# Kernel optimization log

Measured on AMD Instinct MI355X. Metric: run time of the kernel, lower is better.

Reference implementation:

```python
import jax, jax.numpy as jnp
import numpy as np

# Dimensions
B, T, IN = 8, 64, 6       # batch, timesteps, strain components
G = 256                   # grain_num
H = 32                    # hidden_dim (units)
W = 128                   # quadratic block width
OUT = 3                   # output_dim
DEPTH = 4                 # quadratic block depth
SD = H + IN               # start_dim = units + in_channels = 38
EPS = 1e-15


def setup_inputs() -> dict:
    key = jax.random.key(0)
    ks = jax.random.split(key, 24)
    s = 0.08  # xavier-ish scale for width-128 linears
    d = {
        "x": jax.random.normal(ks[0], (B, T, IN), dtype=jnp.float32),
        "init_ori": jax.random.normal(ks[1], (B, G, 3), dtype=jnp.float32),
        # Quadratic block branch A (modlist1): first layer SD->W, then (DEPTH-1) W->W
        "qbA_W0": jax.random.normal(ks[2], (SD, W)) * s,
        "qbA_b0": jnp.zeros((W,), jnp.float32),
        "qbA_Ws": jax.random.normal(ks[3], (DEPTH - 1, W, W)) * s,
        "qbA_bs": jnp.zeros((DEPTH - 1, W), jnp.float32),
        # Quadratic block branch B (modlist2)
        "qbB_W0": jax.random.normal(ks[4], (SD, W)) * s,
        "qbB_b0": jnp.zeros((W,), jnp.float32),
        "qbB_Ws": jax.random.normal(ks[5], (DEPTH - 1, W, W)) * s,
        "qbB_bs": jnp.zeros((DEPTH - 1, W), jnp.float32),
        # fc_alpha: W -> H ; fc_beta (1-layer DNN): W -> H
        "alpha_W": jax.random.normal(ks[6], (W, H)) * s,
        "alpha_b": jnp.zeros((H,), jnp.float32),
        "beta_W": jax.random.normal(ks[7], (W, H)) * s,
        "beta_b": jnp.zeros((H,), jnp.float32),
        # nn_out DNN: layers = [H, 128, 128, OUT], tanh between hidden layers
        "out_W0": jax.random.normal(ks[8], (H, 128)) * s,
        "out_b0": jnp.zeros((128,), jnp.float32),
        "out_W1": jax.random.normal(ks[9], (128, 128)) * s,
        "out_b1": jnp.zeros((128,), jnp.float32),
        "out_W2": jax.random.normal(ks[10], (128, OUT)) * s,
        "out_b2": jnp.zeros((OUT,), jnp.float32),
    }
    return d


def reference(x, init_ori, qbA_W0, qbA_b0, qbA_Ws, qbA_bs,
              qbB_W0, qbB_b0, qbB_Ws, qbB_bs,
              alpha_W, alpha_b, beta_W, beta_b,
              out_W0, out_b0, out_W1, out_b1, out_W2, out_b2):
    b = x.shape[0]
    # h0 = zeros with first 3 hidden channels set to initial orientations
    h0 = jnp.zeros((b, G, H), x.dtype).at[:, :, :3].set(init_ori)

    def step(h, x_t):  # h: [B,G,H], x_t: [B,IN]
        sn = jnp.linalg.norm(x_t, axis=-1, keepdims=True)          # [B,1]
        xn = x_t / (sn + EPS)                                      # normalized strain direction
        z = jnp.concatenate(
            [jnp.broadcast_to(xn[:, None, :], (b, G, IN)), h], axis=-1)  # [B,G,SD]
        # quadratic block: elementwise product of two linear branches
        a = jnp.tanh(z @ qbA_W0 + qbA_b0)
        c = jnp.tanh(z @ qbB_W0 + qbB_b0)
        z = a * c
        for j in range(DEPTH - 1):
            a = z @ qbA_Ws[j] + qbA_bs[j]
            c = z @ qbB_Ws[j] + qbB_bs[j]
            if j < DEPTH - 2:  # tanh on all but the last quadratic layer
                a = jnp.tanh(a)
                c = jnp.tanh(c)
            z = a * c
        q = jnp.tanh(z)                                            # [B,G,W]
        alpha = jnp.exp(q @ alpha_W + alpha_b)                     # [B,G,H]
        beta = jnp.tanh(q @ beta_W + beta_b)                       # [B,G,H]
        decay = jnp.exp(-alpha * sn[:, :, None])                   # exp(-alpha*||strain||)
        h_new = decay * (h - beta) + beta                          # gated state update
        # nn_out DNN [H,128,128,OUT] with tanh hidden activations
        o = jnp.tanh(h_new @ out_W0 + out_b0)
        o = jnp.tanh(o @ out_W1 + out_b1)
        o = o @ out_W2 + out_b2                                    # [B,G,OUT]
        return h_new, o

    _, outs = jax.lax.scan(step, h0, jnp.swapaxes(x, 0, 1))        # outs: [T,B,G,OUT]
    return jnp.transpose(outs, (1, 2, 0, 3))                       # [B,G,T,OUT]
```

## Files before the change

### kernel.cpp

```cpp
#include <hip/hip_runtime.h>

typedef _Float16 f16;
typedef _Float16 f16x4 __attribute__((ext_vector_type(4)));
typedef _Float16 f16x8 __attribute__((ext_vector_type(8)));
typedef float f32x4 __attribute__((ext_vector_type(4)));
typedef unsigned int u32;

#define MFMA16(a,b,c) __builtin_amdgcn_mfma_f32_16x16x32_f16(a,b,c,0,0,0)

#define BAR() asm volatile("s_waitcnt lgkmcnt(0)\n\ts_barrier" ::: "memory")

#define OFF_A0 0
#define OFF_B0 8192
#define OFF_AW 16384
#define OFF_BW 65536
#define OFF_AL 114688
#define OFF_BE 118784
#define OFF_O0 122880
#define OFF_O1 126976
#define OFF_O2 143360
#define PACK_TOTAL 145408
#define OFF_HH 262144

struct PackSrcs { const float* p[9]; };

__global__ __launch_bounds__(256) void pack_all(PackSrcs ps, f16* __restrict__ dst){
  int idx = blockIdx.x*256 + threadIdx.x;
  if (idx >= PACK_TOTAL) return;
  const float* src; int base, Kreal, Nreal, KT;
  if (idx < 16384){
    if (idx < 8192){ src=ps.p[0]; base=0; } else { src=ps.p[1]; base=8192; }
    Kreal=38; Nreal=128; KT=2;
  } else if (idx < 65536){
    int s=(idx-16384)>>14; src=ps.p[2]+s*16384; base=16384+s*16384; Kreal=128; Nreal=128; KT=4;
  } else if (idx < 114688){
    int s=(idx-65536)>>14; src=ps.p[3]+s*16384; base=65536+s*16384; Kreal=128; Nreal=128; KT=4;
  } else if (idx < 122880){
    if (idx<118784){ src=ps.p[4]; base=114688; } else { src=ps.p[5]; base=118784; }
    Kreal=128; Nreal=32; KT=4;
  } else if (idx < 126976){
    src=ps.p[6]; base=122880; Kreal=32; Nreal=128; KT=1;
  } else if (idx < 143360){
    src=ps.p[7]; base=126976; Kreal=128; Nreal=128; KT=4;
  } else {
    src=ps.p[8]; base=143360; Kreal=128; Nreal=3; KT=4;
  }
  int local = idx - base;
  int j = local & 7, lane = (local>>3)&63, rem = local>>9;
  int kt = rem % KT, nt = rem / KT;
  int k = kt*32 + ((lane>>4)<<3) + j;
  int n = nt*16 + (lane&15);
  dst[idx] = (f16)((k<Kreal && n<Nreal) ? src[k*Nreal+n] : 0.f);
}

__device__ __forceinline__ float tanhfast(float x){
  float e = __builtin_amdgcn_exp2f(x * 2.885390082f);
  return 1.f - 2.f*__builtin_amdgcn_rcpf(e + 1.f);
}
__device__ __forceinline__ float expfast(float x){
  return __builtin_amdgcn_exp2f(x * 1.44269504f);
}

__device__ __forceinline__ f16x8 ldW(const f16* wp, int off, int KT, int nt, int kt, int l){
  return *(const f16x8*)(wp + off + (((nt*KT + kt)*64 + l)<<3));
}

template<int LAST>
__device__ __forceinline__ void qphase(const f16* __restrict__ Zi, f16* __restrict__ Zo,
                                       const f16x8 (&WA)[4], const f16x8 (&WB)[4],
                                       const float* __restrict__ bA,
                                       const float* __restrict__ bB,
                                       int l, int d0, int n16){
  f16x8 Bq[4];
#pragma unroll
  for (int kt=0; kt<4; ++kt) Bq[kt] = *(const f16x8*)(Zi + ((kt*64 + l)<<3));
  f32x4 a = *(const f32x4*)(bA + d0);
  f32x4 c = *(const f32x4*)(bB + d0);
#pragma unroll
  for (int kt=0; kt<4; ++kt){
    a = MFMA16(WA[kt], Bq[kt], a);
    c = MFMA16(WB[kt], Bq[kt], c);
  }
  f16x4 z4;
#pragma unroll
  for (int i=0;i<4;++i){
    float z = LAST ? tanhfast(a[i]*c[i]) : tanhfast(a[i])*tanhfast(c[i]);
    z4[i] = (f16)z;
  }
  int kt_o = d0>>5, lane_o = (((d0&31)>>3)<<4) | n16, j0 = d0&7;
  *(f16x4*)(Zo + ((kt_o*64 + lane_o)<<3) + j0) = z4;
}

__global__ __launch_bounds__(512,2)
void lmsc_rec(const float* __restrict__ x, const float* __restrict__ init_ori,
              const f16* __restrict__ wp,
              const float* __restrict__ ba0, const float* __restrict__ bas,
              const float* __restrict__ bb0, const float* __restrict__ bbs,
              const float* __restrict__ b_al, const float* __restrict__ b_be,
              f16* __restrict__ hG)
{
  __shared__ __align__(16) f16 S[2][1024];
  __shared__ __align__(16) f16 Z[2][2048];
  __shared__ float biasA[4][128], biasB[4][128], biasAB[64];
  __shared__ float hbuf[512];
  __shared__ float xnL[64][8];

  const int tid = (int)threadIdx.x;
  const int l = tid & 63, wid = tid >> 6;
  const int n16 = l & 15, rhi = l >> 4;
  const int d0 = (wid<<4) + (rhi<<2);
  const int tile = (int)blockIdx.x, b = tile >> 4, Rbase = tile << 4;

  f16x8 w0A[2], w0B[2];
#pragma unroll
  for (int kt=0;kt<2;++kt){
    w0A[kt] = ldW(wp, OFF_A0, 2, wid, kt, l);
    w0B[kt] = ldW(wp, OFF_B0, 2, wid, kt, l);
  }
  f16x8 wqA[3][4], wqB[3][4];
#pragma unroll
  for (int ly=0;ly<3;++ly)
#pragma unroll
    for (int kt=0;kt<4;++kt){
      wqA[ly][kt] = ldW(wp, OFF_AW + ly*16384, 4, wid, kt, l);
      wqB[ly][kt] = ldW(wp, OFF_BW + ly*16384, 4, wid, kt, l);
    }
  f16x8 wal[4], wbe[4];
  if (wid < 2){
#pragma unroll
    for (int kt=0;kt<4;++kt){
      wal[kt] = ldW(wp, OFF_AL, 4, wid, kt, l);
      wbe[kt] = ldW(wp, OFF_BE, 4, wid, kt, l);
    }
  }

  ((u32*)S)[tid] = 0u; ((u32*)S)[tid+512] = 0u;
  if (tid < 128){
    biasA[0][tid] = ba0[tid]; biasB[0][tid] = bb0[tid];
#pragma unroll
    for (int j=0;j<3;++j){ biasA[1+j][tid] = bas[j*128+tid]; biasB[1+j][tid] = bbs[j*128+tid]; }
  }
  if (tid < 32){ biasAB[tid] = b_al[tid]; biasAB[32+tid] = b_be[tid]; }
  if (tid < 64){
    const float* xp = x + (b*64 + tid)*6;
    float s2 = 0.f;
#pragma unroll
    for (int i=0;i<6;++i) s2 += xp[i]*xp[i];
    float sn = sqrtf(s2);
    float inv = 1.f/(sn + 1e-15f);
#pragma unroll
    for (int i=0;i<6;++i) xnL[tid][i] = xp[i]*inv;
    xnL[tid][6] = sn;
  }
  __syncthreads();
  if (tid < 256){
    int r = tid & 15, cc = tid >> 4;
#pragma unroll
    for (int e=0;e<2;++e){
      int c = cc + e*16;
      float h0 = (c < 3) ? init_ori[(Rbase + r)*3 + c] : 0.f;
      hbuf[c*16 + r] = h0;
      f16 hh = (f16)h0, hl = (f16)(h0 - (float)hh);
      int k = 6 + c;
      int idx = (((k>>5)*64 + (((k&31)>>3)<<4) + r)<<3) + (k&7);
      S[0][idx] = hh; S[1][idx] = hl;
    }
  }
  if (tid < 96){
    int r2 = tid/6, c2 = tid - r2*6;
    float xv = xnL[0][c2];
    f16 xh = (f16)xv, xl = (f16)(xv - (float)xh);
    S[0][(r2<<3)+c2] = xh; S[1][(r2<<3)+c2] = xl;
  }
  __syncthreads();

  for (int t=0; t<64; ++t){
    {
      f16x8 Bh[2], Bl[2];
#pragma unroll
      for (int kt=0;kt<2;++kt){
        Bh[kt] = *(const f16x8*)(&S[0][(kt*64+l)<<3]);
        Bl[kt] = *(const f16x8*)(&S[1][(kt*64+l)<<3]);
      }
      f32x4 aH = *(const f32x4*)(&biasA[0][d0]);
      f32x4 cH = *(const f32x4*)(&biasB[0][d0]);
      f32x4 aL = {0,0,0,0}, cL = {0,0,0,0};
#pragma unroll
      for (int kt=0;kt<2;++kt){
        aH = MFMA16(w0A[kt], Bh[kt], aH); aL = MFMA16(w0A[kt], Bl[kt], aL);
        cH = MFMA16(w0B[kt], Bh[kt], cH); cL = MFMA16(w0B[kt], Bl[kt], cL);
      }
      f16x4 z4;
#pragma unroll
      for (int i=0;i<4;++i)
        z4[i] = (f16)(tanhfast(aH[i]+aL[i]) * tanhfast(cH[i]+cL[i]));
      int kt_o = d0>>5, lane_o = (((d0&31)>>3)<<4) | n16, j0 = d0&7;
      *(f16x4*)(&Z[0][((kt_o*64 + lane_o)<<3) + j0]) = z4;
    }
    BAR();
    qphase<0>(Z[0], Z[1], wqA[0], wqB[0], biasA[1], biasB[1], l, d0, n16);
    BAR();
    qphase<0>(Z[1], Z[0], wqA[1], wqB[1], biasA[2], biasB[2], l, d0, n16);
    BAR();
    qphase<1>(Z[0], Z[1], wqA[2], wqB[2], biasA[3], biasB[3], l, d0, n16);
    BAR();
    if (wid < 2){
      f16x8 q[4];
#pragma unroll
      for (int kt=0;kt<4;++kt) q[kt] = *(const f16x8*)(&Z[1][(kt*64+l)<<3]);
      f32x4 ua = *(const f32x4*)(&biasAB[d0]);
      f32x4 ub = *(const f32x4*)(&biasAB[32+d0]);
#pragma unroll
      for (int kt=0;kt<4;++kt){
        ua = MFMA16(wal[kt], q[kt], ua);
        ub = MFMA16(wbe[kt], q[kt], ub);
      }
      float sn = xnL[t][6];
      int mt = tile*64 + t;
      f16x4 hh4;
#pragma unroll
      for (int i=0;i<4;++i){
        float alv = expfast(fminf(ua[i], 80.f));
        float bev = tanhfast(ub[i]);
        int c = d0 + i;
        float hold = hbuf[c*16 + n16];
        float hn = __builtin_amdgcn_exp2f(-1.44269504f*alv*sn)*(hold - bev) + bev;
        hbuf[c*16 + n16] = hn;
        f16 hh = (f16)hn; hh4[i] = hh;
        if (t < 63){
          f16 hl = (f16)(hn - (float)hh);
          int k = 6 + c;
          int idx = (((k>>5)*64 + (((k&31)>>3)<<4) + n16)<<3) + (k&7);
          S[0][idx] = hh; S[1][idx] = hl;
        }
      }
      int lane_o = ((d0>>3)<<4) | n16;
      *(f16x4*)(hG + mt*512 + lane_o*8 + (d0&7)) = hh4;
    }
    if (t < 63 && tid >= 384 && tid < 480){
      int i2 = tid - 384;
      int r2 = i2/6, c2 = i2 - r2*6;
      float xv = xnL[t+1][c2];
      f16 xh = (f16)xv, xl = (f16)(xv - (float)xh);
      S[0][(r2<<3)+c2] = xh; S[1][(r2<<3)+c2] = xl;
    }
    BAR();
  }
}

__global__ __launch_bounds__(512,4)
void lmsc_out(const f16* __restrict__ wp, const f16* __restrict__ hG,
              const float* __restrict__ bo0, const float* __restrict__ bo1,
              const float* __restrict__ bo2, float* __restrict__ out)
{
  __shared__ __align__(16) f16 o1b[16384];
  __shared__ __align__(16) f16 o2b[16384];
  const int tid=(int)threadIdx.x, l=tid&63, wid=tid>>6;
  const int n16=l&15, rhi=l>>4;
  const int mtb = (int)blockIdx.x * 8;
  f16x8 W0a = ldW(wp, OFF_O0, 1, wid, 0, l);
  f16x8 W1a[4], W2a[4];
#pragma unroll
  for (int kt=0;kt<4;++kt){ W1a[kt]=ldW(wp,OFF_O1,4,wid,kt,l); W2a[kt]=ldW(wp,OFF_O2,4,0,kt,l); }
  const int d0 = wid*16 + rhi*4;
  const f32x4 b0v = *(const f32x4*)(bo0 + d0);
  const f32x4 b1v = *(const f32x4*)(bo1 + d0);
  const int kt_o = d0>>5, lane_o = (((d0&31)>>3)<<4) + n16, j0 = d0&7;
#pragma unroll
  for (int s=0;s<8;++s){
    int mt = mtb + s;
    f16x8 Bh = *(const f16x8*)(hG + ((mt*64+l)<<3));
    f32x4 acc = b0v;
    acc = MFMA16(W0a, Bh, acc);
    f16x4 z4;
#pragma unroll
    for (int i=0;i<4;++i) z4[i] = (f16)tanhfast(acc[i]);
    *(f16x4*)(&o1b[(((s*4+kt_o)*64 + lane_o)<<3) + j0]) = z4;
  }
  __syncthreads();
#pragma unroll
  for (int s=0;s<8;++s){
    f32x4 acc = b1v;
#pragma unroll
    for (int kt=0;kt<4;++kt){
      f16x8 B = *(const f16x8*)(&o1b[((s*4+kt)*64 + l)<<3]);
      acc = MFMA16(W1a[kt], B, acc);
    }
    f16x4 z4;
#pragma unroll
    for (int i=0;i<4;++i) z4[i] = (f16)tanhfast(acc[i]);
    *(f16x4*)(&o2b[(((s*4+kt_o)*64 + lane_o)<<3) + j0]) = z4;
  }
  __syncthreads();
  {
    f32x4 acc = {0,0,0,0};
#pragma unroll
    for (int kt=0;kt<4;++kt){
      f16x8 B = *(const f16x8*)(&o2b[((wid*4+kt)*64 + l)<<3]);
      acc = MFMA16(W2a[kt], B, acc);
    }
    if (l < 16){
      int mt = mtb + wid, grow = (mt>>6)*16 + n16, tt = mt & 63;
#pragma unroll
      for (int i=0;i<3;++i)
        out[(grow*64 + tt)*3 + i] = acc[i] + bo2[i];
    }
  }
}

extern "C" void kernel_launch(void* const* d_in, const int* in_sizes, int n_in,
                              void* d_out, int out_size, void* d_ws, size_t ws_size,
                              hipStream_t stream){
  const float* x        = (const float*)d_in[0];
  const float* init_ori = (const float*)d_in[1];
  f16* wp = (f16*)d_ws;

  PackSrcs ps;
  ps.p[0] = (const float*)d_in[2];
  ps.p[1] = (const float*)d_in[6];
  ps.p[2] = (const float*)d_in[4];
  ps.p[3] = (const float*)d_in[8];
  ps.p[4] = (const float*)d_in[10];
  ps.p[5] = (const float*)d_in[12];
  ps.p[6] = (const float*)d_in[14];
  ps.p[7] = (const float*)d_in[16];
  ps.p[8] = (const float*)d_in[18];
  pack_all<<<(PACK_TOTAL+255)/256, 256, 0, stream>>>(ps, wp);

  lmsc_rec<<<128,512,0,stream>>>(x, init_ori, wp,
      (const float*)d_in[3],  (const float*)d_in[5],
      (const float*)d_in[7],  (const float*)d_in[9],
      (const float*)d_in[11], (const float*)d_in[13],
      wp + OFF_HH);
  lmsc_out<<<1024,512,0,stream>>>(wp, wp + OFF_HH,
      (const float*)d_in[15], (const float*)d_in[17], (const float*)d_in[19],
      (float*)d_out);
}
```

Baseline: 139.7 us.

## Split MFMA accumulation chains, fuse tanh products, keep hidden state in registers

The 4-deep dependent MFMA chains in the quadratic layers and the alpha/beta projection are split into two independent accumulator chains that are summed at the end, which shortens the dependency latency on the serial recurrence path. The product of two tanh values is computed from two exp2 calls and a single reciprocal instead of two reciprocals. The recurrent hidden state moves from an LDS buffer into per-thread registers, removing an LDS read and write each step. Risks include extra VGPR pressure under the 512x2 launch bounds and a slight change in rounding from the exp clamping and the reordered summation.

New measurement: 151.9 us. 8.8% more time.

```diff
diff --git a/kernel.cpp b/kernel.cpp
--- a/kernel.cpp
+++ b/kernel.cpp
@@ -60,6 +60,13 @@
 __device__ __forceinline__ float expfast(float x){
   return __builtin_amdgcn_exp2f(x * 1.44269504f);
 }
+__device__ __forceinline__ float tanh2prod(float a, float c){
+  float pa = __builtin_amdgcn_exp2f(fminf(a*2.885390082f, 60.f));
+  float pc = __builtin_amdgcn_exp2f(fminf(c*2.885390082f, 60.f));
+  float num = (pa-1.f)*(pc-1.f);
+  float den = (pa+1.f)*(pc+1.f);
+  return num * __builtin_amdgcn_rcpf(den);
+}
 
 __device__ __forceinline__ f16x8 ldW(const f16* wp, int off, int KT, int nt, int kt, int l){
   return *(const f16x8*)(wp + off + (((nt*KT + kt)*64 + l)<<3));
@@ -74,17 +81,18 @@
   f16x8 Bq[4];
 #pragma unroll
   for (int kt=0; kt<4; ++kt) Bq[kt] = *(const f16x8*)(Zi + ((kt*64 + l)<<3));
-  f32x4 a = *(const f32x4*)(bA + d0);
-  f32x4 c = *(const f32x4*)(bB + d0);
-#pragma unroll
-  for (int kt=0; kt<4; ++kt){
-    a = MFMA16(WA[kt], Bq[kt], a);
-    c = MFMA16(WB[kt], Bq[kt], c);
-  }
+  f32x4 a0 = *(const f32x4*)(bA + d0);
+  f32x4 c0 = *(const f32x4*)(bB + d0);
+  f32x4 a1 = {0,0,0,0}, c1 = {0,0,0,0};
+  a0 = MFMA16(WA[0], Bq[0], a0); c0 = MFMA16(WB[0], Bq[0], c0);
+  a1 = MFMA16(WA[2], Bq[2], a1); c1 = MFMA16(WB[2], Bq[2], c1);
+  a0 = MFMA16(WA[1], Bq[1], a0); c0 = MFMA16(WB[1], Bq[1], c0);
+  a1 = MFMA16(WA[3], Bq[3], a1); c1 = MFMA16(WB[3], Bq[3], c1);
+  f32x4 a = a0 + a1, c = c0 + c1;
   f16x4 z4;
 #pragma unroll
   for (int i=0;i<4;++i){
-    float z = LAST ? tanhfast(a[i]*c[i]) : tanhfast(a[i])*tanhfast(c[i]);
+    float z = LAST ? tanhfast(a[i]*c[i]) : tanh2prod(a[i], c[i]);
     z4[i] = (f16)z;
   }
   int kt_o = d0>>5, lane_o = (((d0&31)>>3)<<4) | n16, j0 = d0&7;
@@ -102,7 +110,6 @@
   __shared__ __align__(16) f16 S[2][1024];
   __shared__ __align__(16) f16 Z[2][2048];
   __shared__ float biasA[4][128], biasB[4][128], biasAB[64];
-  __shared__ float hbuf[512];
   __shared__ float xnL[64][8];
 
   const int tid = (int)threadIdx.x;
@@ -152,6 +159,14 @@
     for (int i=0;i<6;++i) xnL[tid][i] = xp[i]*inv;
     xnL[tid][6] = sn;
   }
+  float hreg[4] = {0.f,0.f,0.f,0.f};
+  if (wid < 2){
+#pragma unroll
+    for (int i=0;i<4;++i){
+      int c = d0 + i;
+      hreg[i] = (c < 3) ? init_ori[(Rbase + n16)*3 + c] : 0.f;
+    }
+  }
   __syncthreads();
   if (tid < 256){
     int r = tid & 15, cc = tid >> 4;
@@ -159,7 +174,6 @@
     for (int e=0;e<2;++e){
       int c = cc + e*16;
       float h0 = (c < 3) ? init_ori[(Rbase + r)*3 + c] : 0.f;
-      hbuf[c*16 + r] = h0;
       f16 hh = (f16)h0, hl = (f16)(h0 - (float)hh);
       int k = 6 + c;
       int idx = (((k>>5)*64 + (((k&31)>>3)<<4) + r)<<3) + (k&7);
@@ -193,7 +207,7 @@
       f16x4 z4;
 #pragma unroll
       for (int i=0;i<4;++i)
-        z4[i] = (f16)(tanhfast(aH[i]+aL[i]) * tanhfast(cH[i]+cL[i]));
+        z4[i] = (f16)tanh2prod(aH[i]+aL[i], cH[i]+cL[i]);
       int kt_o = d0>>5, lane_o = (((d0&31)>>3)<<4) | n16, j0 = d0&7;
       *(f16x4*)(&Z[0][((kt_o*64 + lane_o)<<3) + j0]) = z4;
     }
@@ -208,13 +222,14 @@
       f16x8 q[4];
 #pragma unroll
       for (int kt=0;kt<4;++kt) q[kt] = *(const f16x8*)(&Z[1][(kt*64+l)<<3]);
-      f32x4 ua = *(const f32x4*)(&biasAB[d0]);
-      f32x4 ub = *(const f32x4*)(&biasAB[32+d0]);
-#pragma unroll
-      for (int kt=0;kt<4;++kt){
-        ua = MFMA16(wal[kt], q[kt], ua);
-        ub = MFMA16(wbe[kt], q[kt], ub);
-      }
+      f32x4 ua0 = *(const f32x4*)(&biasAB[d0]);
+      f32x4 ub0 = *(const f32x4*)(&biasAB[32+d0]);
+      f32x4 ua1 = {0,0,0,0}, ub1 = {0,0,0,0};
+      ua0 = MFMA16(wal[0], q[0], ua0); ub0 = MFMA16(wbe[0], q[0], ub0);
+      ua1 = MFMA16(wal[2], q[2], ua1); ub1 = MFMA16(wbe[2], q[2], ub1);
+      ua0 = MFMA16(wal[1], q[1], ua0); ub0 = MFMA16(wbe[1], q[1], ub0);
+      ua1 = MFMA16(wal[3], q[3], ua1); ub1 = MFMA16(wbe[3], q[3], ub1);
+      f32x4 ua = ua0 + ua1, ub = ub0 + ub1;
       float sn = xnL[t][6];
       int mt = tile*64 + t;
       f16x4 hh4;
@@ -223,9 +238,8 @@
         float alv = expfast(fminf(ua[i], 80.f));
         float bev = tanhfast(ub[i]);
         int c = d0 + i;
-        float hold = hbuf[c*16 + n16];
-        float hn = __builtin_amdgcn_exp2f(-1.44269504f*alv*sn)*(hold - bev) + bev;
-        hbuf[c*16 + n16] = hn;
+        float hn = __builtin_amdgcn_exp2f(-1.44269504f*alv*sn)*(hreg[i] - bev) + bev;
+        hreg[i] = hn;
         f16 hh = (f16)hn; hh4[i] = hh;
         if (t < 63){
           f16 hl = (f16)(hn - (float)hh);
```

## Fuse recurrence and output MLP into one kernel with flag-based producer-consumer overlap

Applied to the files above, without the earlier changes.

Merges the recurrent kernel and the output MLP kernel into one launch of 256 blocks. The first 128 blocks run the recurrence and release a global atomic flag after every 8 timesteps. The other 128 blocks spin on those flags and run the output MLP on each finished chunk while the recurrence continues. This hides the output-MLP work and one launch behind the serial recurrence, but it relies on all 256 blocks being resident at once and adds larger shared memory per block plus the cost of spin-waiting.

After: 171.0 us. 22.5% more time.

```diff
diff --git a/kernel.cpp b/kernel.cpp
--- a/kernel.cpp
+++ b/kernel.cpp
@@ -20,13 +20,15 @@
 #define OFF_O1 126976
 #define OFF_O2 143360
 #define PACK_TOTAL 145408
+#define FLAG_ELEM 153600
 #define OFF_HH 262144
 
 struct PackSrcs { const float* p[9]; };
 
 __global__ __launch_bounds__(256) void pack_all(PackSrcs ps, f16* __restrict__ dst){
   int idx = blockIdx.x*256 + threadIdx.x;
-  if (idx >= PACK_TOTAL) return;
+  if (idx >= PACK_TOTAL + 1024) return;
+  if (idx >= PACK_TOTAL){ ((u32*)(dst + FLAG_ELEM))[idx - PACK_TOTAL] = 0u; return; }
   const float* src; int base, Kreal, Nreal, KT;
   if (idx < 16384){
     if (idx < 8192){ src=ps.p[0]; base=0; } else { src=ps.p[1]; base=8192; }
@@ -92,218 +94,229 @@
 }
 
 __global__ __launch_bounds__(512,2)
-void lmsc_rec(const float* __restrict__ x, const float* __restrict__ init_ori,
-              const f16* __restrict__ wp,
-              const float* __restrict__ ba0, const float* __restrict__ bas,
-              const float* __restrict__ bb0, const float* __restrict__ bbs,
-              const float* __restrict__ b_al, const float* __restrict__ b_be,
-              f16* __restrict__ hG)
+void lmsc_fused(const float* __restrict__ x, const float* __restrict__ init_ori,
+                const f16* __restrict__ wp,
+                const float* __restrict__ ba0, const float* __restrict__ bas,
+                const float* __restrict__ bb0, const float* __restrict__ bbs,
+                const float* __restrict__ b_al, const float* __restrict__ b_be,
+                const float* __restrict__ bo0, const float* __restrict__ bo1,
+                const float* __restrict__ bo2,
+                f16* __restrict__ hG, u32* __restrict__ flags,
+                float* __restrict__ out)
 {
   __shared__ __align__(16) f16 S[2][1024];
   __shared__ __align__(16) f16 Z[2][2048];
   __shared__ float biasA[4][128], biasB[4][128], biasAB[64];
   __shared__ float hbuf[512];
   __shared__ float xnL[64][8];
+  __shared__ __align__(16) f16 o1b[16384];
+  __shared__ __align__(16) f16 o2b[16384];
 
   const int tid = (int)threadIdx.x;
   const int l = tid & 63, wid = tid >> 6;
   const int n16 = l & 15, rhi = l >> 4;
-  const int d0 = (wid<<4) + (rhi<<2);
-  const int tile = (int)blockIdx.x, b = tile >> 4, Rbase = tile << 4;
-
-  f16x8 w0A[2], w0B[2];
-#pragma unroll
-  for (int kt=0;kt<2;++kt){
-    w0A[kt] = ldW(wp, OFF_A0, 2, wid, kt, l);
-    w0B[kt] = ldW(wp, OFF_B0, 2, wid, kt, l);
-  }
-  f16x8 wqA[3][4], wqB[3][4];
-#pragma unroll
-  for (int ly=0;ly<3;++ly)
-#pragma unroll
-    for (int kt=0;kt<4;++kt){
-      wqA[ly][kt] = ldW(wp, OFF_AW + ly*16384, 4, wid, kt, l);
-      wqB[ly][kt] = ldW(wp, OFF_BW + ly*16384, 4, wid, kt, l);
-    }
-  f16x8 wal[4], wbe[4];
-  if (wid < 2){
-#pragma unroll
-    for (int kt=0;kt<4;++kt){
-      wal[kt] = ldW(wp, OFF_AL, 4, wid, kt, l);
-      wbe[kt] = ldW(wp, OFF_BE, 4, wid, kt, l);
-    }
-  }
-
-  ((u32*)S)[tid] = 0u; ((u32*)S)[tid+512] = 0u;
-  if (tid < 128){
-    biasA[0][tid] = ba0[tid]; biasB[0][tid] = bb0[tid];
-#pragma unroll
-    for (int j=0;j<3;++j){ biasA[1+j][tid] = bas[j*128+tid]; biasB[1+j][tid] = bbs[j*128+tid]; }
-  }
-  if (tid < 32){ biasAB[tid] = b_al[tid]; biasAB[32+tid] = b_be[tid]; }
-  if (tid < 64){
-    const float* xp = x + (b*64 + tid)*6;
-    float s2 = 0.f;
-#pragma unroll
-    for (int i=0;i<6;++i) s2 += xp[i]*xp[i];
-    float sn = sqrtf(s2);
-    float inv = 1.f/(sn + 1e-15f);
-#pragma unroll
-    for (int i=0;i<6;++i) xnL[tid][i] = xp[i]*inv;
-    xnL[tid][6] = sn;
-  }
-  __syncthreads();
-  if (tid < 256){
-    int r = tid & 15, cc = tid >> 4;
-#pragma unroll
-    for (int e=0;e<2;++e){
-      int c = cc + e*16;
-      float h0 = (c < 3) ? init_ori[(Rbase + r)*3 + c] : 0.f;
-      hbuf[c*16 + r] = h0;
-      f16 hh = (f16)h0, hl = (f16)(h0 - (float)hh);
-      int k = 6 + c;
-      int idx = (((k>>5)*64 + (((k&31)>>3)<<4) + r)<<3) + (k&7);
-      S[0][idx] = hh; S[1][idx] = hl;
-    }
-  }
-  if (tid < 96){
-    int r2 = tid/6, c2 = tid - r2*6;
-    float xv = xnL[0][c2];
-    f16 xh = (f16)xv, xl = (f16)(xv - (float)xh);
-    S[0][(r2<<3)+c2] = xh; S[1][(r2<<3)+c2] = xl;
-  }
-  __syncthreads();
-
-  for (int t=0; t<64; ++t){
-    {
-      f16x8 Bh[2], Bl[2];
-#pragma unroll
-      for (int kt=0;kt<2;++kt){
-        Bh[kt] = *(const f16x8*)(&S[0][(kt*64+l)<<3]);
-        Bl[kt] = *(const f16x8*)(&S[1][(kt*64+l)<<3]);
-      }
-      f32x4 aH = *(const f32x4*)(&biasA[0][d0]);
-      f32x4 cH = *(const f32x4*)(&biasB[0][d0]);
-      f32x4 aL = {0,0,0,0}, cL = {0,0,0,0};
-#pragma unroll
-      for (int kt=0;kt<2;++kt){
-        aH = MFMA16(w0A[kt], Bh[kt], aH); aL = MFMA16(w0A[kt], Bl[kt], aL);
-        cH = MFMA16(w0B[kt], Bh[kt], cH); cL = MFMA16(w0B[kt], Bl[kt], cL);
-      }
-      f16x4 z4;
-#pragma unroll
-      for (int i=0;i<4;++i)
-        z4[i] = (f16)(tanhfast(aH[i]+aL[i]) * tanhfast(cH[i]+cL[i]));
-      int kt_o = d0>>5, lane_o = (((d0&31)>>3)<<4) | n16, j0 = d0&7;
-      *(f16x4*)(&Z[0][((kt_o*64 + lane_o)<<3) + j0]) = z4;
-    }
-    BAR();
-    qphase<0>(Z[0], Z[1], wqA[0], wqB[0], biasA[1], biasB[1], l, d0, n16);
-    BAR();
-    qphase<0>(Z[1], Z[0], wqA[1], wqB[1], biasA[2], biasB[2], l, d0, n16);
-    BAR();
-    qphase<1>(Z[0], Z[1], wqA[2], wqB[2], biasA[3], biasB[3], l, d0, n16);
-    BAR();
+
+  if (blockIdx.x < 128){
+    const int d0 = (wid<<4) + (rhi<<2);
+    const int tile = (int)blockIdx.x, b = tile >> 4, Rbase = tile << 4;
+
+    f16x8 w0A[2], w0B[2];
+#pragma unroll
+    for (int kt=0;kt<2;++kt){
+      w0A[kt] = ldW(wp, OFF_A0, 2, wid, kt, l);
+      w0B[kt] = ldW(wp, OFF_B0, 2, wid, kt, l);
+    }
+    f16x8 wqA[3][4], wqB[3][4];
+#pragma unroll
+    for (int ly=0;ly<3;++ly)
+#pragma unroll
+      for (int kt=0;kt<4;++kt){
+        wqA[ly][kt] = ldW(wp, OFF_AW + ly*16384, 4, wid, kt, l);
+        wqB[ly][kt] = ldW(wp, OFF_BW + ly*16384, 4, wid, kt, l);
+      }
+    f16x8 wal[4], wbe[4];
     if (wid < 2){
-      f16x8 q[4];
-#pragma unroll
-      for (int kt=0;kt<4;++kt) q[kt] = *(const f16x8*)(&Z[1][(kt*64+l)<<3]);
-      f32x4 ua = *(const f32x4*)(&biasAB[d0]);
-      f32x4 ub = *(const f32x4*)(&biasAB[32+d0]);
 #pragma unroll
       for (int kt=0;kt<4;++kt){
-        ua = MFMA16(wal[kt], q[kt], ua);
-        ub = MFMA16(wbe[kt], q[kt], ub);
-      }
-      float sn = xnL[t][6];
-      int mt = tile*64 + t;
-      f16x4 hh4;
-#pragma unroll
-      for (int i=0;i<4;++i){
-        float alv = expfast(fminf(ua[i], 80.f));
-        float bev = tanhfast(ub[i]);
-        int c = d0 + i;
-        float hold = hbuf[c*16 + n16];
-        float hn = __builtin_amdgcn_exp2f(-1.44269504f*alv*sn)*(hold - bev) + bev;
-        hbuf[c*16 + n16] = hn;
-        f16 hh = (f16)hn; hh4[i] = hh;
-        if (t < 63){
-          f16 hl = (f16)(hn - (float)hh);
-          int k = 6 + c;
-          int idx = (((k>>5)*64 + (((k&31)>>3)<<4) + n16)<<3) + (k&7);
-          S[0][idx] = hh; S[1][idx] = hl;
-        }
-      }
-      int lane_o = ((d0>>3)<<4) | n16;
-      *(f16x4*)(hG + mt*512 + lane_o*8 + (d0&7)) = hh4;
-    }
-    if (t < 63 && tid >= 384 && tid < 480){
-      int i2 = tid - 384;
-      int r2 = i2/6, c2 = i2 - r2*6;
-      float xv = xnL[t+1][c2];
+        wal[kt] = ldW(wp, OFF_AL, 4, wid, kt, l);
+        wbe[kt] = ldW(wp, OFF_BE, 4, wid, kt, l);
+      }
+    }
+
+    ((u32*)S)[tid] = 0u; ((u32*)S)[tid+512] = 0u;
+    if (tid < 128){
+      biasA[0][tid] = ba0[tid]; biasB[0][tid] = bb0[tid];
+#pragma unroll
+      for (int j=0;j<3;++j){ biasA[1+j][tid] = bas[j*128+tid]; biasB[1+j][tid] = bbs[j*128+tid]; }
+    }
+    if (tid < 32){ biasAB[tid] = b_al[tid]; biasAB[32+tid] = b_be[tid]; }
+    if (tid < 64){
+      const float* xp = x + (b*64 + tid)*6;
+      float s2 = 0.f;
+#pragma unroll
+      for (int i=0;i<6;++i) s2 += xp[i]*xp[i];
+      float sn = sqrtf(s2);
+      float inv = 1.f/(sn + 1e-15f);
+#pragma unroll
+      for (int i=0;i<6;++i) xnL[tid][i] = xp[i]*inv;
+      xnL[tid][6] = sn;
+    }
+    __syncthreads();
+    if (tid < 256){
+      int r = tid & 15, cc = tid >> 4;
+#pragma unroll
+      for (int e=0;e<2;++e){
+        int c = cc + e*16;
+        float h0 = (c < 3) ? init_ori[(Rbase + r)*3 + c] : 0.f;
+        hbuf[c*16 + r] = h0;
+        f16 hh = (f16)h0, hl = (f16)(h0 - (float)hh);
+        int k = 6 + c;
+        int idx = (((k>>5)*64 + (((k&31)>>3)<<4) + r)<<3) + (k&7);
+        S[0][idx] = hh; S[1][idx] = hl;
+      }
+    }
+    if (tid < 96){
+      int r2 = tid/6, c2 = tid - r2*6;
+      float xv = xnL[0][c2];
       f16 xh = (f16)xv, xl = (f16)(xv - (float)xh);
       S[0][(r2<<3)+c2] = xh; S[1][(r2<<3)+c2] = xl;
     }
-    BAR();
-  }
-}
-
-__global__ __launch_bounds__(512,4)
-void lmsc_out(const f16* __restrict__ wp, const f16* __restrict__ hG,
-              const float* __restrict__ bo0, const float* __restrict__ bo1,
-              const float* __restrict__ bo2, float* __restrict__ out)
-{
-  __shared__ __align__(16) f16 o1b[16384];
-  __shared__ __align__(16) f16 o2b[16384];
-  const int tid=(int)threadIdx.x, l=tid&63, wid=tid>>6;
-  const int n16=l&15, rhi=l>>4;
-  const int mtb = (int)blockIdx.x * 8;
-  f16x8 W0a = ldW(wp, OFF_O0, 1, wid, 0, l);
-  f16x8 W1a[4], W2a[4];
-#pragma unroll
-  for (int kt=0;kt<4;++kt){ W1a[kt]=ldW(wp,OFF_O1,4,wid,kt,l); W2a[kt]=ldW(wp,OFF_O2,4,0,kt,l); }
-  const int d0 = wid*16 + rhi*4;
-  const f32x4 b0v = *(const f32x4*)(bo0 + d0);
-  const f32x4 b1v = *(const f32x4*)(bo1 + d0);
-  const int kt_o = d0>>5, lane_o = (((d0&31)>>3)<<4) + n16, j0 = d0&7;
-#pragma unroll
-  for (int s=0;s<8;++s){
-    int mt = mtb + s;
-    f16x8 Bh = *(const f16x8*)(hG + ((mt*64+l)<<3));
-    f32x4 acc = b0v;
-    acc = MFMA16(W0a, Bh, acc);
-    f16x4 z4;
-#pragma unroll
-    for (int i=0;i<4;++i) z4[i] = (f16)tanhfast(acc[i]);
-    *(f16x4*)(&o1b[(((s*4+kt_o)*64 + lane_o)<<3) + j0]) = z4;
-  }
-  __syncthreads();
-#pragma unroll
-  for (int s=0;s<8;++s){
-    f32x4 acc = b1v;
-#pragma unroll
-    for (int kt=0;kt<4;++kt){
-      f16x8 B = *(const f16x8*)(&o1b[((s*4+kt)*64 + l)<<3]);
-      acc = MFMA16(W1a[kt], B, acc);
-    }
-    f16x4 z4;
-#pragma unroll
-    for (int i=0;i<4;++i) z4[i] = (f16)tanhfast(acc[i]);
-    *(f16x4*)(&o2b[(((s*4+kt_o)*64 + lane_o)<<3) + j0]) = z4;
-  }
-  __syncthreads();
-  {
-    f32x4 acc = {0,0,0,0};
-#pragma unroll
-    for (int kt=0;kt<4;++kt){
-      f16x8 B = *(const f16x8*)(&o2b[((wid*4+kt)*64 + l)<<3]);
-      acc = MFMA16(W2a[kt], B, acc);
-    }
-    if (l < 16){
-      int mt = mtb + wid, grow = (mt>>6)*16 + n16, tt = mt & 63;
-#pragma unroll
-      for (int i=0;i<3;++i)
-        out[(grow*64 + tt)*3 + i] = acc[i] + bo2[i];
+    __syncthreads();
+
+    for (int t=0; t<64; ++t){
+      {
+        f16x8 Bh[2], Bl[2];
+#pragma unroll
+        for (int kt=0;kt<2;++kt){
+          Bh[kt] = *(const f16x8*)(&S[0][(kt*64+l)<<3]);
+          Bl[kt] = *(const f16x8*)(&S[1][(kt*64+l)<<3]);
+        }
+        f32x4 aH = *(const f32x4*)(&biasA[0][d0]);
+        f32x4 cH = *(const f32x4*)(&biasB[0][d0]);
+        f32x4 aL = {0,0,0,0}, cL = {0,0,0,0};
+#pragma unroll
+        for (int kt=0;kt<2;++kt){
+          aH = MFMA16(w0A[kt], Bh[kt], aH); aL = MFMA16(w0A[kt], Bl[kt], aL);
+          cH = MFMA16(w0B[kt], Bh[kt], cH); cL = MFMA16(w0B[kt], Bl[kt], cL);
+        }
+        f16x4 z4;
+#pragma unroll
+        for (int i=0;i<4;++i)
+          z4[i] = (f16)(tanhfast(aH[i]+aL[i]) * tanhfast(cH[i]+cL[i]));
+        int kt_o = d0>>5, lane_o = (((d0&31)>>3)<<4) | n16, j0 = d0&7;
+        *(f16x4*)(&Z[0][((kt_o*64 + lane_o)<<3) + j0]) = z4;
+      }
+      BAR();
+      qphase<0>(Z[0], Z[1], wqA[0], wqB[0], biasA[1], biasB[1], l, d0, n16);
+      BAR();
+      qphase<0>(Z[1], Z[0], wqA[1], wqB[1], biasA[2], biasB[2], l, d0, n16);
+      BAR();
+      qphase<1>(Z[0], Z[1], wqA[2], wqB[2], biasA[3], biasB[3], l, d0, n16);
+      BAR();
+      if (wid < 2){
+        f16x8 q[4];
+#pragma unroll
+        for (int kt=0;kt<4;++kt) q[kt] = *(const f16x8*)(&Z[1][(kt*64+l)<<3]);
+        f32x4 ua = *(const f32x4*)(&biasAB[d0]);
+        f32x4 ub = *(const f32x4*)(&biasAB[32+d0]);
+#pragma unroll
+        for (int kt=0;kt<4;++kt){
+          ua = MFMA16(wal[kt], q[kt], ua);
+          ub = MFMA16(wbe[kt], q[kt], ub);
+        }
+        float sn = xnL[t][6];
+        int mt = tile*64 + t;
+        f16x4 hh4;
+#pragma unroll
+        for (int i=0;i<4;++i){
+          float alv = expfast(fminf(ua[i], 80.f));
+          float bev = tanhfast(ub[i]);
+          int c = d0 + i;
+          float hold = hbuf[c*16 + n16];
+          float hn = __builtin_amdgcn_exp2f(-1.44269504f*alv*sn)*(hold - bev) + bev;
+          hbuf[c*16 + n16] = hn;
+          f16 hh = (f16)hn; hh4[i] = hh;
+          if (t < 63){
+            f16 hl = (f16)(hn - (float)hh);
+            int k = 6 + c;
+            int idx = (((k>>5)*64 + (((k&31)>>3)<<4) + n16)<<3) + (k&7);
+            S[0][idx] = hh; S[1][idx] = hl;
+          }
+        }
+        int lane_o = ((d0>>3)<<4) | n16;
+        *(f16x4*)(hG + mt*512 + lane_o*8 + (d0&7)) = hh4;
+        if ((t & 7) == 7 && l == 0)
+          __hip_atomic_fetch_add(&flags[(tile<<3) + (t>>3)], 1u,
+                                 __ATOMIC_RELEASE, __HIP_MEMORY_SCOPE_AGENT);
+      }
+      if (t < 63 && tid >= 384 && tid < 480){
+        int i2 = tid - 384;
+        int r2 = i2/6, c2 = i2 - r2*6;
+        float xv = xnL[t+1][c2];
+        f16 xh = (f16)xv, xl = (f16)(xv - (float)xh);
+        S[0][(r2<<3)+c2] = xh; S[1][(r2<<3)+c2] = xl;
+      }
+      BAR();
+    }
+  } else {
+    const int r = (int)blockIdx.x - 128;
+    f16x8 W0a = ldW(wp, OFF_O0, 1, wid, 0, l);
+    f16x8 W1a[4], W2a[4];
+#pragma unroll
+    for (int kt=0;kt<4;++kt){ W1a[kt]=ldW(wp,OFF_O1,4,wid,kt,l); W2a[kt]=ldW(wp,OFF_O2,4,0,kt,l); }
+    const int d0 = wid*16 + rhi*4;
+    const f32x4 b0v = *(const f32x4*)(bo0 + d0);
+    const f32x4 b1v = *(const f32x4*)(bo1 + d0);
+    const int kt_o = d0>>5, lane_o = (((d0&31)>>3)<<4) + n16, j0 = d0&7;
+    u32* fl = flags + (r<<3);
+
+    for (int oct=0; oct<8; ++oct){
+      if (tid == 0){
+        while (__hip_atomic_load(&fl[oct], __ATOMIC_ACQUIRE, __HIP_MEMORY_SCOPE_AGENT) < 2u)
+          __builtin_amdgcn_s_sleep(4);
+      }
+      __syncthreads();
+      const int mtb = (r<<6) + (oct<<3);
+#pragma unroll
+      for (int s=0;s<8;++s){
+        int mt = mtb + s;
+        f16x8 Bh = *(const f16x8*)(hG + ((mt*64+l)<<3));
+        f32x4 acc = b0v;
+        acc = MFMA16(W0a, Bh, acc);
+        f16x4 z4;
+#pragma unroll
+        for (int i=0;i<4;++i) z4[i] = (f16)tanhfast(acc[i]);
+        *(f16x4*)(&o1b[(((s*4+kt_o)*64 + lane_o)<<3) + j0]) = z4;
+      }
+      __syncthreads();
+#pragma unroll
+      for (int s=0;s<8;++s){
+        f32x4 acc = b1v;
+#pragma unroll
+        for (int kt=0;kt<4;++kt){
+          f16x8 B = *(const f16x8*)(&o1b[((s*4+kt)*64 + l)<<3]);
+          acc = MFMA16(W1a[kt], B, acc);
+        }
+        f16x4 z4;
+#pragma unroll
+        for (int i=0;i<4;++i) z4[i] = (f16)tanhfast(acc[i]);
+        *(f16x4*)(&o2b[(((s*4+kt_o)*64 + lane_o)<<3) + j0]) = z4;
+      }
+      __syncthreads();
+      {
+        f32x4 acc = {0,0,0,0};
+#pragma unroll
+        for (int kt=0;kt<4;++kt){
+          f16x8 B = *(const f16x8*)(&o2b[((wid*4+kt)*64 + l)<<3]);
+          acc = MFMA16(W2a[kt], B, acc);
+        }
+        if (l < 16){
+          int mt = mtb + wid, grow = (mt>>6)*16 + n16, tt = mt & 63;
+#pragma unroll
+          for (int i=0;i<3;++i)
+            out[(grow*64 + tt)*3 + i] = acc[i] + bo2[i];
+        }
+      }
     }
   }
 }
@@ -314,6 +327,7 @@
   const float* x        = (const float*)d_in[0];
   const float* init_ori = (const float*)d_in[1];
   f16* wp = (f16*)d_ws;
+  u32* flags = (u32*)(wp + FLAG_ELEM);
 
   PackSrcs ps;
   ps.p[0] = (const float*)d_in[2];
@@ -325,14 +339,12 @@
   ps.p[6] = (const float*)d_in[14];
   ps.p[7] = (const float*)d_in[16];
   ps.p[8] = (const float*)d_in[18];
-  pack_all<<<(PACK_TOTAL+255)/256, 256, 0, stream>>>(ps, wp);
-
-  lmsc_rec<<<128,512,0,stream>>>(x, init_ori, wp,
+  pack_all<<<(PACK_TOTAL+1024+255)/256, 256, 0, stream>>>(ps, wp);
+
+  lmsc_fused<<<256,512,0,stream>>>(x, init_ori, wp,
       (const float*)d_in[3],  (const float*)d_in[5],
       (const float*)d_in[7],  (const float*)d_in[9],
       (const float*)d_in[11], (const float*)d_in[13],
-      wp + OFF_HH);
-  lmsc_out<<<1024,512,0,stream>>>(wp, wp + OFF_HH,
       (const float*)d_in[15], (const float*)d_in[17], (const float*)d_in[19],
-      (float*)d_out);
-}
+      wp + OFF_HH, flags, (float*)d_out);
+}
```

## Precompute input-strain contribution to first quadratic layer outside the recurrence

Applied to the files above, without the earlier changes.

The x-dependent part of the first quadratic layer (6 strain inputs times W0 plus bias) does not depend on the hidden state. It is now precomputed for all 64 timesteps in fp32 into shared-memory tables before the time loop. The packed first-layer weights now hold only the 32 hidden rows, so the per-step MFMA K dimension drops from 64 to 32 and half the MFMAs go away. The per-step x staging into shared memory is removed and the h writes are vectorised. The cost is 64 KB of extra LDS, which may reduce occupancy below the two blocks per CU requested by the launch bounds.

Result: faster. 135.6 us (-2.9%).

```diff
diff --git a/kernel.cpp b/kernel.cpp
--- a/kernel.cpp
+++ b/kernel.cpp
@@ -50,6 +50,7 @@
   int kt = rem % KT, nt = rem / KT;
   int k = kt*32 + ((lane>>4)<<3) + j;
   int n = nt*16 + (lane&15);
+  if (base < 16384) k = (k < 32) ? (k + 6) : 99;
   dst[idx] = (f16)((k<Kreal && n<Nreal) ? src[k*Nreal+n] : 0.f);
 }
 
@@ -94,16 +95,19 @@
 __global__ __launch_bounds__(512,2)
 void lmsc_rec(const float* __restrict__ x, const float* __restrict__ init_ori,
               const f16* __restrict__ wp,
+              const float* __restrict__ w0Araw, const float* __restrict__ w0Braw,
               const float* __restrict__ ba0, const float* __restrict__ bas,
               const float* __restrict__ bb0, const float* __restrict__ bbs,
               const float* __restrict__ b_al, const float* __restrict__ b_be,
               f16* __restrict__ hG)
 {
-  __shared__ __align__(16) f16 S[2][1024];
+  __shared__ __align__(16) f16 S[2][512];
   __shared__ __align__(16) f16 Z[2][2048];
   __shared__ float biasA[4][128], biasB[4][128], biasAB[64];
   __shared__ float hbuf[512];
   __shared__ float xnL[64][8];
+  __shared__ __align__(16) float UA[64][128];
+  __shared__ __align__(16) float UC[64][128];
 
   const int tid = (int)threadIdx.x;
   const int l = tid & 63, wid = tid >> 6;
@@ -111,12 +115,8 @@
   const int d0 = (wid<<4) + (rhi<<2);
   const int tile = (int)blockIdx.x, b = tile >> 4, Rbase = tile << 4;
 
-  f16x8 w0A[2], w0B[2];
-#pragma unroll
-  for (int kt=0;kt<2;++kt){
-    w0A[kt] = ldW(wp, OFF_A0, 2, wid, kt, l);
-    w0B[kt] = ldW(wp, OFF_B0, 2, wid, kt, l);
-  }
+  f16x8 w0A = ldW(wp, OFF_A0, 2, wid, 0, l);
+  f16x8 w0B = ldW(wp, OFF_B0, 2, wid, 0, l);
   f16x8 wqA[3][4], wqB[3][4];
 #pragma unroll
   for (int ly=0;ly<3;++ly)
@@ -134,7 +134,6 @@
     }
   }
 
-  ((u32*)S)[tid] = 0u; ((u32*)S)[tid+512] = 0u;
   if (tid < 128){
     biasA[0][tid] = ba0[tid]; biasB[0][tid] = bb0[tid];
 #pragma unroll
@@ -153,6 +152,25 @@
     xnL[tid][6] = sn;
   }
   __syncthreads();
+  {
+    const int dim = tid & 127, t0 = (tid >> 7) << 4;
+    float wA[6], wC[6];
+#pragma unroll
+    for (int k=0;k<6;++k){ wA[k] = w0Araw[k*128+dim]; wC[k] = w0Braw[k*128+dim]; }
+    const float bA_ = biasA[0][dim], bC_ = biasB[0][dim];
+#pragma unroll
+    for (int tt=0;tt<16;++tt){
+      int t = t0 + tt;
+      float aA = bA_, aC = bC_;
+#pragma unroll
+      for (int k=0;k<6;++k){
+        float xv = xnL[t][k];
+        aA += xv * wA[k];
+        aC += xv * wC[k];
+      }
+      UA[t][dim] = aA; UC[t][dim] = aC;
+    }
+  }
   if (tid < 256){
     int r = tid & 15, cc = tid >> 4;
 #pragma unroll
@@ -161,35 +179,21 @@
       float h0 = (c < 3) ? init_ori[(Rbase + r)*3 + c] : 0.f;
       hbuf[c*16 + r] = h0;
       f16 hh = (f16)h0, hl = (f16)(h0 - (float)hh);
-      int k = 6 + c;
-      int idx = (((k>>5)*64 + (((k&31)>>3)<<4) + r)<<3) + (k&7);
+      int idx = ((((c>>3)<<4) | r)<<3) + (c&7);
       S[0][idx] = hh; S[1][idx] = hl;
     }
-  }
-  if (tid < 96){
-    int r2 = tid/6, c2 = tid - r2*6;
-    float xv = xnL[0][c2];
-    f16 xh = (f16)xv, xl = (f16)(xv - (float)xh);
-    S[0][(r2<<3)+c2] = xh; S[1][(r2<<3)+c2] = xl;
   }
   __syncthreads();
 
   for (int t=0; t<64; ++t){
     {
-      f16x8 Bh[2], Bl[2];
-#pragma unroll
-      for (int kt=0;kt<2;++kt){
-        Bh[kt] = *(const f16x8*)(&S[0][(kt*64+l)<<3]);
-        Bl[kt] = *(const f16x8*)(&S[1][(kt*64+l)<<3]);
-      }
-      f32x4 aH = *(const f32x4*)(&biasA[0][d0]);
-      f32x4 cH = *(const f32x4*)(&biasB[0][d0]);
+      f16x8 Bh = *(const f16x8*)(&S[0][l<<3]);
+      f16x8 Bl = *(const f16x8*)(&S[1][l<<3]);
+      f32x4 aH = *(const f32x4*)(&UA[t][d0]);
+      f32x4 cH = *(const f32x4*)(&UC[t][d0]);
       f32x4 aL = {0,0,0,0}, cL = {0,0,0,0};
-#pragma unroll
-      for (int kt=0;kt<2;++kt){
-        aH = MFMA16(w0A[kt], Bh[kt], aH); aL = MFMA16(w0A[kt], Bl[kt], aL);
-        cH = MFMA16(w0B[kt], Bh[kt], cH); cL = MFMA16(w0B[kt], Bl[kt], cL);
-      }
+      aH = MFMA16(w0A, Bh, aH); aL = MFMA16(w0A, Bl, aL);
+      cH = MFMA16(w0B, Bh, cH); cL = MFMA16(w0B, Bl, cL);
       f16x4 z4;
 #pragma unroll
       for (int i=0;i<4;++i)
@@ -217,7 +221,7 @@
       }
       float sn = xnL[t][6];
       int mt = tile*64 + t;
-      f16x4 hh4;
+      f16x4 hh4, hl4;
 #pragma unroll
       for (int i=0;i<4;++i){
         float alv = expfast(fminf(ua[i], 80.f));
@@ -226,23 +230,15 @@
         float hold = hbuf[c*16 + n16];
         float hn = __builtin_amdgcn_exp2f(-1.44269504f*alv*sn)*(hold - bev) + bev;
         hbuf[c*16 + n16] = hn;
-        f16 hh = (f16)hn; hh4[i] = hh;
-        if (t < 63){
-          f16 hl = (f16)(hn - (float)hh);
-          int k = 6 + c;
-          int idx = (((k>>5)*64 + (((k&31)>>3)<<4) + n16)<<3) + (k&7);
-          S[0][idx] = hh; S[1][idx] = hl;
-        }
+        f16 hh = (f16)hn; hh4[i] = hh; hl4[i] = (f16)(hn - (float)hh);
+      }
+      if (t < 63){
+        int sb = ((((d0>>3)<<4) | n16)<<3) + (d0&7);
+        *(f16x4*)(&S[0][sb]) = hh4;
+        *(f16x4*)(&S[1][sb]) = hl4;
       }
       int lane_o = ((d0>>3)<<4) | n16;
       *(f16x4*)(hG + mt*512 + lane_o*8 + (d0&7)) = hh4;
-    }
-    if (t < 63 && tid >= 384 && tid < 480){
-      int i2 = tid - 384;
-      int r2 = i2/6, c2 = i2 - r2*6;
-      float xv = xnL[t+1][c2];
-      f16 xh = (f16)xv, xl = (f16)(xv - (float)xh);
-      S[0][(r2<<3)+c2] = xh; S[1][(r2<<3)+c2] = xl;
     }
     BAR();
   }
@@ -328,6 +324,7 @@
   pack_all<<<(PACK_TOTAL+255)/256, 256, 0, stream>>>(ps, wp);
 
   lmsc_rec<<<128,512,0,stream>>>(x, init_ori, wp,
+      (const float*)d_in[2],  (const float*)d_in[6],
       (const float*)d_in[3],  (const float*)d_in[5],
       (const float*)d_in[7],  (const float*)d_in[9],
       (const float*)d_in[11], (const float*)d_in[13],
```
